# Kernel tuning notes

Measured on AMD Instinct MI355X. Metric: run time of the kernel, lower is better.

The kernel has to match this reference:

```python
import jax, jax.numpy as jnp
import numpy as np

B, S, D, H = 4, 2048, 512, 8
HD = D // H  # head dim = 64


def setup_inputs() -> dict:
    key = jax.random.key(0)
    ks = jax.random.split(key, 7)
    s = 0.02
    return {
        "X": jax.random.normal(ks[0], (B, S, D), dtype=jnp.float32),
        "Y": jax.random.normal(ks[1], (B, S, D), dtype=jnp.float32),
        "Z": jax.random.normal(ks[2], (B, S, D), dtype=jnp.float32),
        # weights stored as [in, out] (torch Linear weight transposed)
        "Wq": jax.random.normal(ks[3], (D, D), dtype=jnp.float32) * s,
        "Wk": jax.random.normal(ks[4], (D, D), dtype=jnp.float32) * s,
        "Wv": jax.random.normal(ks[5], (D, D), dtype=jnp.float32) * s,  # dead in original forward
        "Wo": jax.random.normal(ks[6], (D, D), dtype=jnp.float32) * s,
    }


def _split_heads(t):
    # [B, S, D] -> [B, H, S, HD]
    return t.reshape(B, S, H, HD).transpose(0, 2, 1, 3)


def reference(X, Y, Z, Wq, Wk, Wv, Wo):
    q = _split_heads(X @ Wq)
    k = _split_heads(Y @ Wk)
    # NOTE: original module (faithfully) uses W_o for the value projection; W_v is unused.
    v = _split_heads(Z @ Wo)
    scores = jnp.einsum("bhqd,bhkd->bhqk", q, k) / jnp.sqrt(jnp.float32(HD))
    # sigmoid(s) > 0.5  <=>  s > 0 (sigmoid strictly monotone); keep score else 0
    scores = jnp.where(scores > 0, scores, jnp.float32(0))
    attn = jax.nn.softmax(scores, axis=-1)
    out = jnp.einsum("bhqk,bhkd->bhqd", attn, v)  # dropout inactive at eval
    out = out.transpose(0, 2, 1, 3).reshape(B, S, D)  # merge heads
    return out @ Wo
```

## Files before the change

kernel.cpp:

```cpp
#include <hip/hip_runtime.h>
#include <math.h>

#define S_LEN 2048
#define DIM   512
#define M_TOT 8192
#define NCH   (S_LEN / 64)

typedef __attribute__((ext_vector_type(8))) short bf16x8;
typedef __attribute__((ext_vector_type(4))) short bf16x4;
typedef __attribute__((ext_vector_type(4))) float f32x4;

#define MFMA(a, b, c) __builtin_amdgcn_mfma_f32_16x16x32_bf16((a), (b), (c), 0, 0, 0)

#define QSCALE 0.18033688011112042f

__device__ __forceinline__ short f2b(float x) {
    union { float f; unsigned u; } v; v.f = x;
    unsigned r = v.u + 0x7FFFu + ((v.u >> 16) & 1u);
    return (short)(r >> 16);
}

__device__ __forceinline__ unsigned cvtpk(float a, float b) {
    unsigned r;
    asm("v_cvt_pk_bf16_f32 %0, %1, %2" : "=v"(r) : "v"(a), "v"(b));
    return r;
}

__device__ __forceinline__ bf16x8 cvt8(float4 lo, float4 hi) {
    union { unsigned u[4]; bf16x8 v; } o;
    o.u[0] = cvtpk(lo.x, lo.y);
    o.u[1] = cvtpk(lo.z, lo.w);
    o.u[2] = cvtpk(hi.x, hi.y);
    o.u[3] = cvtpk(hi.z, hi.w);
    return o.v;
}

__device__ __forceinline__ float fast_exp2(float x) {
#if __has_builtin(__builtin_amdgcn_exp2f)
    return __builtin_amdgcn_exp2f(x);
#else
    return __expf(x * 0.693147180559945f);
#endif
}

__global__ __launch_bounds__(256) void prep_wt(const float* Wq, const float* Wk, const float* Wo,
                                               short* Wtq, short* Wtk, short* Wto) {
    const int zi = blockIdx.z;
    const float* W = zi == 0 ? Wq : zi == 1 ? Wk : Wo;
    short*      Wt = zi == 0 ? Wtq : zi == 1 ? Wtk : Wto;
    const float sc = zi == 0 ? QSCALE : 1.0f;
    __shared__ short Ts[64 * 72];
    const int t = threadIdx.x;
    const int k0 = blockIdx.x * 64, n0 = blockIdx.y * 64;
    #pragma unroll
    for (int it = 0; it < 4; ++it) {
        const int r = (t >> 4) + 16 * it;
        const int cq = t & 15;
        float4 v = *(const float4*)&W[(size_t)(k0 + r) * DIM + n0 + cq * 4];
        Ts[(4 * cq + 0) * 72 + r] = f2b(v.x * sc);
        Ts[(4 * cq + 1) * 72 + r] = f2b(v.y * sc);
        Ts[(4 * cq + 2) * 72 + r] = f2b(v.z * sc);
        Ts[(4 * cq + 3) * 72 + r] = f2b(v.w * sc);
    }
    __syncthreads();
    #pragma unroll
    for (int it = 0; it < 2; ++it) {
        const int n = (t >> 3) + 32 * it;
        const int sg = t & 7;
        *(bf16x8*)&Wt[(size_t)(n0 + n) * DIM + k0 + sg * 8] = *(const bf16x8*)&Ts[n * 72 + sg * 8];
    }
}

__global__ __launch_bounds__(256) void proj_gemm(const float* __restrict__ X,
                                                 const float* __restrict__ Y,
                                                 const float* __restrict__ Z,
                                                 const short* __restrict__ Wtq,
                                                 const short* __restrict__ Wtk,
                                                 const short* __restrict__ Wto,
                                                 short* __restrict__ Qb,
                                                 short* __restrict__ Kb,
                                                 short* __restrict__ Vt) {
    const int zi = blockIdx.z;
    const float* A  = zi == 0 ? X : zi == 1 ? Y : Z;
    const short* Bw = zi == 0 ? Wtq : zi == 1 ? Wtk : Wto;

    __shared__ short As[128 * 40];
    __shared__ short Bs[128 * 40];
    const int tid = threadIdx.x;
    const int w = tid >> 6, ln = tid & 63, l15 = ln & 15, quad = ln >> 4;
    const int m0 = blockIdx.x * 128, n0 = blockIdx.y * 128;
    const int wm = (w & 1) * 64, wn = (w >> 1) * 64;

    const int r0 = tid >> 2, r1 = r0 + 64;
    const int sg = tid & 3;
    const float* ap0 = A  + (size_t)(m0 + r0) * DIM + sg * 8;
    const float* ap1 = A  + (size_t)(m0 + r1) * DIM + sg * 8;
    const short* bp0 = Bw + (size_t)(n0 + r0) * DIM + sg * 8;
    const short* bp1 = Bw + (size_t)(n0 + r1) * DIM + sg * 8;

    float4 a0l = *(const float4*)ap0, a0h = *(const float4*)(ap0 + 4);
    float4 a1l = *(const float4*)ap1, a1h = *(const float4*)(ap1 + 4);
    bf16x8 b0 = *(const bf16x8*)bp0, b1 = *(const bf16x8*)bp1;

    f32x4 acc[4][4] = {};

    for (int k0 = 0; k0 < DIM; k0 += 32) {
        __syncthreads();
        *(bf16x8*)&As[r0 * 40 + sg * 8] = cvt8(a0l, a0h);
        *(bf16x8*)&As[r1 * 40 + sg * 8] = cvt8(a1l, a1h);
        *(bf16x8*)&Bs[r0 * 40 + sg * 8] = b0;
        *(bf16x8*)&Bs[r1 * 40 + sg * 8] = b1;
        __syncthreads();
        const int kn = (k0 + 32 < DIM) ? k0 + 32 : 0;
        a0l = *(const float4*)(ap0 + kn); a0h = *(const float4*)(ap0 + kn + 4);
        a1l = *(const float4*)(ap1 + kn); a1h = *(const float4*)(ap1 + kn + 4);
        b0 = *(const bf16x8*)(bp0 + kn); b1 = *(const bf16x8*)(bp1 + kn);

        bf16x8 af[4], bf[4];
        #pragma unroll
        for (int mf = 0; mf < 4; ++mf) af[mf] = *(const bf16x8*)&As[(wm + 16 * mf + l15) * 40 + quad * 8];
        #pragma unroll
        for (int nf = 0; nf < 4; ++nf) bf[nf] = *(const bf16x8*)&Bs[(wn + 16 * nf + l15) * 40 + quad * 8];
        #pragma unroll
        for (int mf = 0; mf < 4; ++mf)
            #pragma unroll
            for (int nf = 0; nf < 4; ++nf)
                acc[mf][nf] = MFMA(af[mf], bf[nf], acc[mf][nf]);
    }

    if (zi < 2) {
        short* C = zi == 0 ? Qb : Kb;
        #pragma unroll
        for (int mf = 0; mf < 4; ++mf)
            #pragma unroll
            for (int nf = 0; nf < 4; ++nf)
                #pragma unroll
                for (int r = 0; r < 4; ++r)
                    C[(size_t)(m0 + wm + 16 * mf + 4 * quad + r) * DIM + n0 + wn + 16 * nf + l15] =
                        f2b(acc[mf][nf][r]);
    } else {
        #pragma unroll
        for (int mf = 0; mf < 4; ++mf)
            #pragma unroll
            for (int nf = 0; nf < 4; ++nf) {
                const int col = n0 + wn + 16 * nf + l15;
                const int h = col >> 6, hd = col & 63;
                const int row0_ = m0 + wm + 16 * mf + 4 * quad;
                const int bb = row0_ >> 11, s0 = row0_ & 2047;
                bf16x4 o = { f2b(acc[mf][nf][0]), f2b(acc[mf][nf][1]),
                             f2b(acc[mf][nf][2]), f2b(acc[mf][nf][3]) };
                *(bf16x4*)&Vt[((size_t)((bb * 8 + h) * 64 + hd)) * S_LEN + s0] = o;
            }
    }
}

__global__ __launch_bounds__(256) void out_gemm(const short* __restrict__ Ob,
                                                const short* __restrict__ Wto,
                                                float* __restrict__ Cout) {
    __shared__ short As[64 * 40];
    __shared__ short Bs[64 * 40];
    const int tid = threadIdx.x;
    const int w = tid >> 6, ln = tid & 63, l15 = ln & 15, quad = ln >> 4;

    const int f = blockIdx.x;
    const int swz = ((f & 7) << 7) | (f >> 3);
    const int m0 = (swz >> 3) * 64, n0 = (swz & 7) * 64;
    const int wm = (w & 1) * 32, wn = (w >> 1) * 32;

    const int row = tid >> 2;
    const int sg = tid & 3;
    const short* ap = Ob  + (size_t)(m0 + row) * DIM + sg * 8;
    const short* bp = Wto + (size_t)(n0 + row) * DIM + sg * 8;

    bf16x8 a0 = *(const bf16x8*)ap, b0 = *(const bf16x8*)bp;

    f32x4 acc[2][2] = {};

    for (int k0 = 0; k0 < DIM; k0 += 32) {
        __syncthreads();
        *(bf16x8*)&As[row * 40 + sg * 8] = a0;
        *(bf16x8*)&Bs[row * 40 + sg * 8] = b0;
        __syncthreads();
        const int kn = (k0 + 32 < DIM) ? k0 + 32 : 0;
        a0 = *(const bf16x8*)(ap + kn); b0 = *(const bf16x8*)(bp + kn);

        bf16x8 af[2], bf[2];
        #pragma unroll
        for (int mf = 0; mf < 2; ++mf) af[mf] = *(const bf16x8*)&As[(wm + 16 * mf + l15) * 40 + quad * 8];
        #pragma unroll
        for (int nf = 0; nf < 2; ++nf) bf[nf] = *(const bf16x8*)&Bs[(wn + 16 * nf + l15) * 40 + quad * 8];
        #pragma unroll
        for (int mf = 0; mf < 2; ++mf)
            #pragma unroll
            for (int nf = 0; nf < 2; ++nf)
                acc[mf][nf] = MFMA(af[mf], bf[nf], acc[mf][nf]);
    }
    #pragma unroll
    for (int mf = 0; mf < 2; ++mf)
        #pragma unroll
        for (int nf = 0; nf < 2; ++nf)
            #pragma unroll
            for (int r = 0; r < 4; ++r)
                Cout[(size_t)(m0 + wm + 16 * mf + 4 * quad + r) * DIM + n0 + wn + 16 * nf + l15] =
                    acc[mf][nf][r];
}

__global__ __launch_bounds__(256) void attn_mfma(const short* __restrict__ Qb,
                                                 const short* __restrict__ Kb,
                                                 const short* __restrict__ Vtg,
                                                 short* __restrict__ Ob) {
    __shared__ short Ks[64 * 72];
    __shared__ short Vs[64 * 72];
    __shared__ short Es[4][16 * 72];

    const int tid = threadIdx.x;
    const int w = tid >> 6, ln = tid & 63, l15 = ln & 15, quad = ln >> 4;

    const int f = blockIdx.x;
    const int swz = ((f & 7) << 7) | (f >> 3);
    const int qt0 = (swz & 31) * 64;
    const int bh  = swz >> 5;
    const int b = bh >> 3, h = bh & 7;
    const size_t tokbase = (size_t)b * S_LEN;

    bf16x8 qf[2];
    #pragma unroll
    for (int ks = 0; ks < 2; ++ks)
        qf[ks] = *(const bf16x8*)&Qb[(tokbase + qt0 + 16 * w + l15) * DIM +
                                     h * 64 + 32 * ks + 8 * quad];

    const int srow = tid >> 3, ssg = tid & 7;
    const short* kbase = Kb  + (tokbase + srow) * DIM + h * 64 + ssg * 8;
    const short* vbase = Vtg + ((size_t)bh * 64 + srow) * S_LEN + ssg * 8;

    bf16x8 k0r = *(const bf16x8*)kbase;
    bf16x8 k1r = *(const bf16x8*)(kbase + (size_t)32 * DIM);
    bf16x8 v0r = *(const bf16x8*)vbase;
    bf16x8 v1r = *(const bf16x8*)(vbase + (size_t)32 * S_LEN);

    f32x4 oacc[4] = {};
    f32x4 d4 = {0.f, 0.f, 0.f, 0.f};

    for (int kc = 0; kc < NCH; ++kc) {
        *(bf16x8*)&Ks[srow * 72 + ssg * 8] = k0r;
        *(bf16x8*)&Ks[(srow + 32) * 72 + ssg * 8] = k1r;
        *(bf16x8*)&Vs[srow * 72 + ssg * 8] = v0r;
        *(bf16x8*)&Vs[(srow + 32) * 72 + ssg * 8] = v1r;
        __syncthreads();
        if (kc + 1 < NCH) {
            const size_t ko = (size_t)(kc + 1) * 64 * DIM;
            const size_t vo = (size_t)(kc + 1) * 64;
            k0r = *(const bf16x8*)(kbase + ko);
            k1r = *(const bf16x8*)(kbase + ko + (size_t)32 * DIM);
            v0r = *(const bf16x8*)(vbase + vo);
            v1r = *(const bf16x8*)(vbase + vo + (size_t)32 * S_LEN);
        }

        f32x4 sacc[4];
        __builtin_amdgcn_s_setprio(1);
        #pragma unroll
        for (int mf = 0; mf < 4; ++mf) {
            bf16x8 ka = *(const bf16x8*)&Ks[(16 * mf + l15) * 72 + 8 * quad];
            bf16x8 kb = *(const bf16x8*)&Ks[(16 * mf + l15) * 72 + 32 + 8 * quad];
            f32x4 s = {0.f, 0.f, 0.f, 0.f};
            s = MFMA(ka, qf[0], s);
            s = MFMA(kb, qf[1], s);
            sacc[mf] = s;
        }
        __builtin_amdgcn_s_setprio(0);

        short* Esw = &Es[w][0];
        #pragma unroll
        for (int mf = 0; mf < 4; ++mf) {
            const float e0 = fast_exp2(fmaxf(sacc[mf][0], 0.f));
            const float e1 = fast_exp2(fmaxf(sacc[mf][1], 0.f));
            const float e2 = fast_exp2(fmaxf(sacc[mf][2], 0.f));
            const float e3 = fast_exp2(fmaxf(sacc[mf][3], 0.f));
            d4[0] += e0; d4[1] += e1; d4[2] += e2; d4[3] += e3;
            uint2 p;
            p.x = cvtpk(e0, e1);
            p.y = cvtpk(e2, e3);
            *(uint2*)&Esw[l15 * 72 + 16 * mf + 4 * quad] = p;
        }

        bf16x8 e0 = *(const bf16x8*)&Esw[l15 * 72 + 8 * quad];
        bf16x8 e1 = *(const bf16x8*)&Esw[l15 * 72 + 32 + 8 * quad];
        __builtin_amdgcn_s_setprio(1);
        #pragma unroll
        for (int nf2 = 0; nf2 < 4; ++nf2) {
            bf16x8 vf0 = *(const bf16x8*)&Vs[(16 * nf2 + l15) * 72 + 8 * quad];
            bf16x8 vf1 = *(const bf16x8*)&Vs[(16 * nf2 + l15) * 72 + 32 + 8 * quad];
            oacc[nf2] = MFMA(e0, vf0, oacc[nf2]);
            oacc[nf2] = MFMA(e1, vf1, oacc[nf2]);
        }
        __builtin_amdgcn_s_setprio(0);
        __syncthreads();
    }

    float dsum = (d4[0] + d4[1]) + (d4[2] + d4[3]);
    dsum += __shfl_xor(dsum, 16);
    dsum += __shfl_xor(dsum, 32);
    const float dinv = 1.0f / dsum;

    #pragma unroll
    for (int r = 0; r < 4; ++r) {
        const float di = __shfl(dinv, 4 * quad + r);
        const size_t rowaddr = (tokbase + qt0 + 16 * w + 4 * quad + r) * DIM + h * 64;
        #pragma unroll
        for (int nf2 = 0; nf2 < 4; ++nf2)
            Ob[rowaddr + 16 * nf2 + l15] = f2b(oacc[nf2][r] * di);
    }
}

extern "C" void kernel_launch(void* const* d_in, const int* in_sizes, int n_in,
                              void* d_out, int out_size, void* d_ws, size_t ws_size,
                              hipStream_t stream) {
    const float* X  = (const float*)d_in[0];
    const float* Y  = (const float*)d_in[1];
    const float* Z  = (const float*)d_in[2];
    const float* Wq = (const float*)d_in[3];
    const float* Wk = (const float*)d_in[4];
    const float* Wo = (const float*)d_in[6];

    char* p = (char*)d_ws;
    const size_t MD = (size_t)M_TOT * DIM;
    short* Qb  = (short*)p; p += MD * 2;
    short* Kb  = (short*)p; p += MD * 2;
    short* Vt  = (short*)p; p += MD * 2;
    short* Ob  = (short*)p; p += MD * 2;
    short* Wtq = (short*)p; p += (size_t)DIM * DIM * 2;
    short* Wtk = (short*)p; p += (size_t)DIM * DIM * 2;
    short* Wto = (short*)p; p += (size_t)DIM * DIM * 2;

    prep_wt<<<dim3(8, 8, 3), 256, 0, stream>>>(Wq, Wk, Wo, Wtq, Wtk, Wto);
    proj_gemm<<<dim3(64, 4, 3), 256, 0, stream>>>(X, Y, Z, Wtq, Wtk, Wto, Qb, Kb, Vt);
    attn_mfma<<<dim3(1024), 256, 0, stream>>>(Qb, Kb, Vt, Ob);
    out_gemm<<<dim3(1024), 256, 0, stream>>>(Ob, Wto, (float*)d_out);
}
```

Before: 203.8 us.

## Switch attention to 32x32 MFMA, 128-query tiles, register P, double-buffered K/V

Rewrites the attention kernel around 32x32x16 bf16 MFMA. Each wave now owns 32 query rows, so a block covers 128 queries and only 512 blocks are launched. The exponentiated scores stay in registers as the A operand of the PV product, which removes the per-wave LDS round trip for P. K and V tiles are double-buffered in LDS with a two-chunk-ahead register prefetch, and V is stored with an interleaved column order so it matches the P fragment layout. The cost is higher register pressure, more LDS, and half as many blocks for the machine to spread across CUs.

```diff
diff --git a/kernel.cpp b/kernel.cpp
--- a/kernel.cpp
+++ b/kernel.cpp
@@ -9,8 +9,10 @@
 typedef __attribute__((ext_vector_type(8))) short bf16x8;
 typedef __attribute__((ext_vector_type(4))) short bf16x4;
 typedef __attribute__((ext_vector_type(4))) float f32x4;
-
-#define MFMA(a, b, c) __builtin_amdgcn_mfma_f32_16x16x32_bf16((a), (b), (c), 0, 0, 0)
+typedef __attribute__((ext_vector_type(16))) float f32x16;
+
+#define MFMA(a, b, c)   __builtin_amdgcn_mfma_f32_16x16x32_bf16((a), (b), (c), 0, 0, 0)
+#define MFMA32(a, b, c) __builtin_amdgcn_mfma_f32_32x32x16_bf16((a), (b), (c), 0, 0, 0)
 
 #define QSCALE 0.18033688011112042f
 
@@ -209,107 +211,128 @@
                                                  const short* __restrict__ Kb,
                                                  const short* __restrict__ Vtg,
                                                  short* __restrict__ Ob) {
-    __shared__ short Ks[64 * 72];
-    __shared__ short Vs[64 * 72];
-    __shared__ short Es[4][16 * 72];
+    __shared__ short Ks[2][64 * 72];
+    __shared__ short Vs[2][64 * 72];
+    __shared__ float Ds[4][32];
 
     const int tid = threadIdx.x;
-    const int w = tid >> 6, ln = tid & 63, l15 = ln & 15, quad = ln >> 4;
+    const int w = tid >> 6, ln = tid & 63, n31 = ln & 31, hL = ln >> 5;
 
     const int f = blockIdx.x;
-    const int swz = ((f & 7) << 7) | (f >> 3);
-    const int qt0 = (swz & 31) * 64;
-    const int bh  = swz >> 5;
+    const int swz = ((f & 7) << 6) | (f >> 3);
+    const int qt0 = (swz & 15) * 128;
+    const int bh  = swz >> 4;
     const int b = bh >> 3, h = bh & 7;
     const size_t tokbase = (size_t)b * S_LEN;
 
-    bf16x8 qf[2];
-    #pragma unroll
-    for (int ks = 0; ks < 2; ++ks)
-        qf[ks] = *(const bf16x8*)&Qb[(tokbase + qt0 + 16 * w + l15) * DIM +
-                                     h * 64 + 32 * ks + 8 * quad];
-
-    const int srow = tid >> 3, ssg = tid & 7;
-    const short* kbase = Kb  + (tokbase + srow) * DIM + h * 64 + ssg * 8;
-    const short* vbase = Vtg + ((size_t)bh * 64 + srow) * S_LEN + ssg * 8;
-
-    bf16x8 k0r = *(const bf16x8*)kbase;
-    bf16x8 k1r = *(const bf16x8*)(kbase + (size_t)32 * DIM);
-    bf16x8 v0r = *(const bf16x8*)vbase;
-    bf16x8 v1r = *(const bf16x8*)(vbase + (size_t)32 * S_LEN);
-
-    f32x4 oacc[4] = {};
+    const int q0w = qt0 + 32 * w;
+    bf16x8 qf[4];
+    #pragma unroll
+    for (int dk = 0; dk < 4; ++dk)
+        qf[dk] = *(const bf16x8*)&Qb[(tokbase + q0w + n31) * DIM + h * 64 + 16 * dk + 8 * hL];
+
+    const int srow = tid >> 2, sg = tid & 3;
+    const short* kbase = Kb  + (tokbase + srow) * DIM + h * 64 + sg * 16;
+    const short* vbase = Vtg + ((size_t)bh * 64 + srow) * S_LEN;
+
+    union b8split { bf16x8 v; struct { bf16x4 lo, hi; } s; };
+
+    bf16x8 kr0, kr1;
+    b8split vrA, vrB;
+
+    f32x16 oacc[2] = {};
     f32x4 d4 = {0.f, 0.f, 0.f, 0.f};
 
+    kr0 = *(const bf16x8*)kbase;       kr1 = *(const bf16x8*)(kbase + 8);
+    vrA.v = *(const bf16x8*)(vbase + 8 * sg);
+    vrB.v = *(const bf16x8*)(vbase + 32 + 8 * sg);
+    *(bf16x8*)&Ks[0][srow * 72 + sg * 16]     = kr0;
+    *(bf16x8*)&Ks[0][srow * 72 + sg * 16 + 8] = kr1;
+    {
+        short* vrow = &Vs[0][srow * 72 + 16 * sg];
+        *(bf16x4*)&vrow[0]  = vrA.s.lo;  *(bf16x4*)&vrow[8]  = vrA.s.hi;
+        *(bf16x4*)&vrow[4]  = vrB.s.lo;  *(bf16x4*)&vrow[12] = vrB.s.hi;
+    }
+    kr0 = *(const bf16x8*)(kbase + (size_t)64 * DIM);
+    kr1 = *(const bf16x8*)(kbase + (size_t)64 * DIM + 8);
+    vrA.v = *(const bf16x8*)(vbase + 64 + 8 * sg);
+    vrB.v = *(const bf16x8*)(vbase + 64 + 32 + 8 * sg);
+    __syncthreads();
+
     for (int kc = 0; kc < NCH; ++kc) {
-        *(bf16x8*)&Ks[srow * 72 + ssg * 8] = k0r;
-        *(bf16x8*)&Ks[(srow + 32) * 72 + ssg * 8] = k1r;
-        *(bf16x8*)&Vs[srow * 72 + ssg * 8] = v0r;
-        *(bf16x8*)&Vs[(srow + 32) * 72 + ssg * 8] = v1r;
-        __syncthreads();
+        const int cur = kc & 1;
         if (kc + 1 < NCH) {
-            const size_t ko = (size_t)(kc + 1) * 64 * DIM;
-            const size_t vo = (size_t)(kc + 1) * 64;
-            k0r = *(const bf16x8*)(kbase + ko);
-            k1r = *(const bf16x8*)(kbase + ko + (size_t)32 * DIM);
-            v0r = *(const bf16x8*)(vbase + vo);
-            v1r = *(const bf16x8*)(vbase + vo + (size_t)32 * S_LEN);
+            *(bf16x8*)&Ks[cur ^ 1][srow * 72 + sg * 16]     = kr0;
+            *(bf16x8*)&Ks[cur ^ 1][srow * 72 + sg * 16 + 8] = kr1;
+            short* vrow = &Vs[cur ^ 1][srow * 72 + 16 * sg];
+            *(bf16x4*)&vrow[0]  = vrA.s.lo;  *(bf16x4*)&vrow[8]  = vrA.s.hi;
+            *(bf16x4*)&vrow[4]  = vrB.s.lo;  *(bf16x4*)&vrow[12] = vrB.s.hi;
         }
-
-        f32x4 sacc[4];
+        if (kc + 2 < NCH) {
+            const size_t ko = (size_t)(kc + 2) * 64 * DIM;
+            const size_t vo = (size_t)(kc + 2) * 64;
+            kr0 = *(const bf16x8*)(kbase + ko);
+            kr1 = *(const bf16x8*)(kbase + ko + 8);
+            vrA.v = *(const bf16x8*)(vbase + vo + 8 * sg);
+            vrB.v = *(const bf16x8*)(vbase + vo + 32 + 8 * sg);
+        }
+
+        f32x16 sacc[2] = {};
         __builtin_amdgcn_s_setprio(1);
         #pragma unroll
-        for (int mf = 0; mf < 4; ++mf) {
-            bf16x8 ka = *(const bf16x8*)&Ks[(16 * mf + l15) * 72 + 8 * quad];
-            bf16x8 kb = *(const bf16x8*)&Ks[(16 * mf + l15) * 72 + 32 + 8 * quad];
-            f32x4 s = {0.f, 0.f, 0.f, 0.f};
-            s = MFMA(ka, qf[0], s);
-            s = MFMA(kb, qf[1], s);
-            sacc[mf] = s;
+        for (int kt = 0; kt < 2; ++kt)
+            #pragma unroll
+            for (int dk = 0; dk < 4; ++dk) {
+                bf16x8 ka = *(const bf16x8*)&Ks[cur][(32 * kt + n31) * 72 + 16 * dk + 8 * hL];
+                sacc[kt] = MFMA32(ka, qf[dk], sacc[kt]);
+            }
+        __builtin_amdgcn_s_setprio(0);
+
+        unsigned cp[16];
+        #pragma unroll
+        for (int kt = 0; kt < 2; ++kt)
+            #pragma unroll
+            for (int p = 0; p < 8; ++p) {
+                const float e0 = fast_exp2(fmaxf(sacc[kt][2 * p], 0.f));
+                const float e1 = fast_exp2(fmaxf(sacc[kt][2 * p + 1], 0.f));
+                d4[p & 3] += e0 + e1;
+                cp[8 * kt + p] = cvtpk(e0, e1);
+            }
+
+        __builtin_amdgcn_s_setprio(1);
+        #pragma unroll
+        for (int m = 0; m < 4; ++m) {
+            union { unsigned u[4]; bf16x8 v; } pu;
+            pu.u[0] = cp[2 * m];     pu.u[1] = cp[2 * m + 1];
+            pu.u[2] = cp[2 * m + 8]; pu.u[3] = cp[2 * m + 9];
+            #pragma unroll
+            for (int nt = 0; nt < 2; ++nt) {
+                bf16x8 vb = *(const bf16x8*)&Vs[cur][(32 * nt + n31) * 72 + 16 * m + 8 * hL];
+                oacc[nt] = MFMA32(pu.v, vb, oacc[nt]);
+            }
         }
         __builtin_amdgcn_s_setprio(0);
-
-        short* Esw = &Es[w][0];
-        #pragma unroll
-        for (int mf = 0; mf < 4; ++mf) {
-            const float e0 = fast_exp2(fmaxf(sacc[mf][0], 0.f));
-            const float e1 = fast_exp2(fmaxf(sacc[mf][1], 0.f));
-            const float e2 = fast_exp2(fmaxf(sacc[mf][2], 0.f));
-            const float e3 = fast_exp2(fmaxf(sacc[mf][3], 0.f));
-            d4[0] += e0; d4[1] += e1; d4[2] += e2; d4[3] += e3;
-            uint2 p;
-            p.x = cvtpk(e0, e1);
-            p.y = cvtpk(e2, e3);
-            *(uint2*)&Esw[l15 * 72 + 16 * mf + 4 * quad] = p;
+        __syncthreads();
+    }
+
+    float dtot = (d4[0] + d4[1]) + (d4[2] + d4[3]);
+    dtot += __shfl_xor(dtot, 32);
+    const float dinv = 1.0f / dtot;
+    if (ln < 32) Ds[w][n31] = dinv;
+    __syncthreads();
+    f32x4 dv[4];
+    #pragma unroll
+    for (int g = 0; g < 4; ++g)
+        dv[g] = *(const f32x4*)&Ds[w][8 * g + 4 * hL];
+
+    #pragma unroll
+    for (int nt = 0; nt < 2; ++nt)
+        #pragma unroll
+        for (int r = 0; r < 16; ++r) {
+            const int qb = 32 * w + 4 * hL + 8 * (r >> 2) + (r & 3);
+            Ob[(tokbase + qt0 + qb) * DIM + h * 64 + 32 * nt + n31] =
+                f2b(oacc[nt][r] * dv[r >> 2][r & 3]);
         }
-
-        bf16x8 e0 = *(const bf16x8*)&Esw[l15 * 72 + 8 * quad];
-        bf16x8 e1 = *(const bf16x8*)&Esw[l15 * 72 + 32 + 8 * quad];
-        __builtin_amdgcn_s_setprio(1);
-        #pragma unroll
-        for (int nf2 = 0; nf2 < 4; ++nf2) {
-            bf16x8 vf0 = *(const bf16x8*)&Vs[(16 * nf2 + l15) * 72 + 8 * quad];
-            bf16x8 vf1 = *(const bf16x8*)&Vs[(16 * nf2 + l15) * 72 + 32 + 8 * quad];
-            oacc[nf2] = MFMA(e0, vf0, oacc[nf2]);
-            oacc[nf2] = MFMA(e1, vf1, oacc[nf2]);
-        }
-        __builtin_amdgcn_s_setprio(0);
-        __syncthreads();
-    }
-
-    float dsum = (d4[0] + d4[1]) + (d4[2] + d4[3]);
-    dsum += __shfl_xor(dsum, 16);
-    dsum += __shfl_xor(dsum, 32);
-    const float dinv = 1.0f / dsum;
-
-    #pragma unroll
-    for (int r = 0; r < 4; ++r) {
-        const float di = __shfl(dinv, 4 * quad + r);
-        const size_t rowaddr = (tokbase + qt0 + 16 * w + 4 * quad + r) * DIM + h * 64;
-        #pragma unroll
-        for (int nf2 = 0; nf2 < 4; ++nf2)
-            Ob[rowaddr + 16 * nf2 + l15] = f2b(oacc[nf2][r] * di);
-    }
 }
 
 extern "C" void kernel_launch(void* const* d_in, const int* in_sizes, int n_in,
@@ -334,6 +357,6 @@
 
     prep_wt<<<dim3(8, 8, 3), 256, 0, stream>>>(Wq, Wk, Wo, Wtq, Wtk, Wto);
     proj_gemm<<<dim3(64, 4, 3), 256, 0, stream>>>(X, Y, Z, Wtq, Wtk, Wto, Qb, Kb, Vt);
-    attn_mfma<<<dim3(1024), 256, 0, stream>>>(Qb, Kb, Vt, Ob);
+    attn_mfma<<<dim3(512), 256, 0, stream>>>(Qb, Kb, Vt, Ob);
     out_gemm<<<dim3(1024), 256, 0, stream>>>(Ob, Wto, (float*)d_out);
 }
```

Result: faster. 193.7 us (-5.0%).
